# Optimization experiments

Hardware: AMD Instinct MI355X
Metric: run time of the kernel (lower is better)

## Reference

```python
import jax, jax.numpy as jnp
import numpy as np

B, R, C, S = 4, 64, 64, 32
V, E, H, L = 30000, 128, 128, 2


def setup_inputs() -> dict:
    key = jax.random.key(0)
    ks = jax.random.split(key, 8)
    return {
        "x": jax.random.randint(ks[0], (B, R, C, S), 0, V),
        "embed": jax.random.normal(ks[1], (V, E), jnp.float32) * 0.02,
        "W_ih": jax.random.normal(ks[2], (L, H, H), jnp.float32) * 0.05,
        "W_hh": jax.random.normal(ks[3], (L, H, H), jnp.float32) * 0.05,
        "b_ih": jax.random.normal(ks[4], (L, H), jnp.float32) * 0.05,
        "b_hh": jax.random.normal(ks[5], (L, H), jnp.float32) * 0.05,
        "pred_W": jax.random.normal(ks[6], (1, 2 * H), jnp.float32) * 0.05,
        "pred_b": jax.random.normal(ks[7], (1,), jnp.float32) * 0.05,
    }


def _rnn_last(x_seq, W_ih, W_hh, b_ih, b_hh):
    """Multi-layer elman RNN (relu), batch_first. x_seq: [N,S,E] -> last hidden of top layer [N,H]."""
    N = x_seq.shape[0]
    inp = x_seq
    for l in range(W_ih.shape[0]):  # small fixed layer loop
        Wi, Wh, bi, bh = W_ih[l], W_hh[l], b_ih[l], b_hh[l]
        # precompute input projection for all timesteps: [N,S,H]
        pre = jnp.einsum('nse,he->nsh', inp, Wi) + bi

        def step(h, p_t):
            h = jax.nn.relu(p_t + h @ Wh.T + bh)
            return h, h

        h0 = jnp.zeros((N, Wh.shape[0]), inp.dtype)
        _, hs = jax.lax.scan(step, h0, jnp.swapaxes(pre, 0, 1))  # [S,N,H]
        inp = jnp.swapaxes(hs, 0, 1)  # [N,S,H]
    return inp[:, -1, :]


def reference(x, embed, W_ih, W_hh, b_ih, b_hh, pred_W, pred_b):
    Bb, Rr, Cc, Ss = x.shape
    emb = embed[x]  # [B,R,C,S,E]  (dropout is identity in eval mode)
    h = _rnn_last(emb.reshape(Bb * Rr * Cc, Ss, emb.shape[-1]), W_ih, W_hh, b_ih, b_hh)
    h = h.reshape(Bb, Rr, Cc, -1)  # per-cell hidden; h_n[-1] == output[:,-1,:] of top layer
    # H_global[cell] = sum over same-row cells (excl self) + same-col cells (excl self)
    Hg = h.sum(axis=2, keepdims=True) + h.sum(axis=1, keepdims=True) - 2.0 * h
    feat = jnp.concatenate([h, Hg], axis=-1)  # [B,R,C,2H]
    return (feat @ pred_W.T + pred_b)[..., 0]  # [B,R,C]
```

## Files before the change

### kernel.cpp

```cpp
#include <hip/hip_runtime.h>
#include <hip/hip_bf16.h>


typedef __attribute__((ext_vector_type(8))) short short8;
typedef __attribute__((ext_vector_type(4))) float f32x4;
typedef __attribute__((ext_vector_type(2))) unsigned int u32x2;
typedef __attribute__((ext_vector_type(4))) unsigned int u32x4;

#define Hd 128
#define Sd 32
#define VROWS 30000

__device__ __forceinline__ unsigned short f2b(float f) {
  __hip_bfloat16 h = __float2bfloat16(f);
  return reinterpret_cast<unsigned short&>(h);
}
__device__ __forceinline__ unsigned int pack2(float a, float b) {
  return (unsigned int)f2b(a) | ((unsigned int)f2b(b) << 16);
}
__device__ __forceinline__ float blo(unsigned int u) { return __uint_as_float(u << 16); }
__device__ __forceinline__ float bhi(unsigned int u) { return __uint_as_float(u & 0xffff0000u); }

__device__ __forceinline__ f32x4 mfma16(short8 a, short8 b, f32x4 c) {
  return __builtin_amdgcn_mfma_f32_16x16x32_bf16(a, b, c, 0, 0, 0);
}

__device__ __forceinline__ short8 load_row8_bf16(const float* __restrict__ p) {
  const float4* q = reinterpret_cast<const float4*>(p);
  float4 a = q[0], b = q[1];
  short8 s;
  s[0] = (short)f2b(a.x); s[1] = (short)f2b(a.y);
  s[2] = (short)f2b(a.z); s[3] = (short)f2b(a.w);
  s[4] = (short)f2b(b.x); s[5] = (short)f2b(b.y);
  s[6] = (short)f2b(b.z); s[7] = (short)f2b(b.w);
  return s;
}

__global__ __launch_bounds__(256, 1) void k_t1p(const float* __restrict__ embed,
                                                const float* __restrict__ W_ih,
                                                const float* __restrict__ b_ih,
                                                const float* __restrict__ b_hh,
                                                unsigned int* __restrict__ T1p) {
  const int tid = threadIdx.x, lane = tid & 63, wid = tid >> 6;
  const int l15 = lane & 15, lg = lane >> 4;
  const int gw = blockIdx.x * 4 + wid;

  short8 Wf[8][4];
  f32x4 biasD[8];
#pragma unroll
  for (int m = 0; m < 8; ++m) {
#pragma unroll
    for (int kt = 0; kt < 4; ++kt)
      Wf[m][kt] = load_row8_bf16(W_ih + (16 * m + l15) * Hd + 32 * kt + 8 * lg);
    const float4 bi = *reinterpret_cast<const float4*>(b_ih + 16 * m + 4 * lg);
    const float4 bh = *reinterpret_cast<const float4*>(b_hh + 16 * m + 4 * lg);
    biasD[m] = (f32x4){bi.x + bh.x, bi.y + bh.y, bi.z + bh.z, bi.w + bh.w};
  }

  for (int tt = gw; tt < 1875; tt += 1024) {
    const int v = tt * 16 + l15;
    short8 Ef[4];
#pragma unroll
    for (int kt = 0; kt < 4; ++kt)
      Ef[kt] = load_row8_bf16(embed + (size_t)v * Hd + 32 * kt + 8 * lg);
    f32x4 acc[8];
#pragma unroll
    for (int m = 0; m < 8; ++m) acc[m] = biasD[m];
#pragma unroll
    for (int kt = 0; kt < 4; ++kt)
#pragma unroll
      for (int m = 0; m < 8; ++m) acc[m] = mfma16(Wf[m][kt], Ef[kt], acc[m]);
    unsigned int dw[16];
#pragma unroll
    for (int m = 0; m < 8; ++m) {
      dw[2 * m]     = pack2(acc[m][0], acc[m][1]);
      dw[2 * m + 1] = pack2(acc[m][2], acc[m][3]);
    }
    unsigned int* dst = T1p + (size_t)v * 64 + lg * 16;
#pragma unroll
    for (int j = 0; j < 4; ++j)
      *reinterpret_cast<u32x4*>(dst + 4 * j) =
          (u32x4){dw[4 * j], dw[4 * j + 1], dw[4 * j + 2], dw[4 * j + 3]};
  }
}

__global__ __launch_bounds__(256, 2) void k_rnn(
    const int* __restrict__ x, const unsigned int* __restrict__ T1p,
    const float* __restrict__ W_ih, const float* __restrict__ W_hh,
    const float* __restrict__ b_ih, const float* __restrict__ b_hh,
    const float* __restrict__ pred_W, float* __restrict__ sbuf) {
  __shared__ alignas(16) unsigned char slab[2][8192];
  __shared__ int xs[32 * 33 + 16];
  __shared__ float sred[4][32][2];

  const int tid = threadIdx.x, lane = tid & 63, ws = tid >> 6;
  const int l15 = lane & 15, lg = lane >> 4;
  const int seq0 = blockIdx.x * 32;

#pragma unroll
  for (int k = 0; k < 4; ++k) {
    int e = tid + k * 256;
    xs[(e >> 5) * 33 + (e & 31)] = x[(size_t)seq0 * Sd + e];
  }
  if (tid < 32) xs[tid * 33 + 32] = 0;
  __syncthreads();

  const int s0 = l15, s1 = l15 + 16;
  const int jbase = 16 * lg + 4 * ws;

  u32x2 t1q[2][2];
  {
    int i0 = xs[s0 * 33 + 0], i1 = xs[s1 * 33 + 0];
    const u32x2* p0 = reinterpret_cast<const u32x2*>(T1p + (size_t)i0 * 64 + jbase);
    const u32x2* p1 = reinterpret_cast<const u32x2*>(T1p + (size_t)i1 * 64 + jbase);
    t1q[0][0] = p0[0]; t1q[0][1] = p0[1];
    t1q[1][0] = p1[0]; t1q[1][1] = p1[1];
  }

  short8 Wh0[2][4], Wi1[2][4], Wh1[2][4];
#pragma unroll
  for (int mt = 0; mt < 2; ++mt)
#pragma unroll
    for (int kt = 0; kt < 4; ++kt) {
      const int ro = (32 * ws + 16 * mt + l15) * Hd + 32 * kt + 8 * lg;
      Wh0[mt][kt] = load_row8_bf16(W_hh + ro);
      Wi1[mt][kt] = load_row8_bf16(W_ih + 16384 + ro);
      Wh1[mt][kt] = load_row8_bf16(W_hh + 16384 + ro);
    }
  u32x2 bsumP[2];
#pragma unroll
  for (int mt = 0; mt < 2; ++mt) {
    const float4 bi = *reinterpret_cast<const float4*>(b_ih + Hd + 32 * ws + 16 * mt + 4 * lg);
    const float4 bh = *reinterpret_cast<const float4*>(b_hh + Hd + 32 * ws + 16 * mt + 4 * lg);
    bsumP[mt][0] = pack2(bi.x + bh.x, bi.y + bh.y);
    bsumP[mt][1] = pack2(bi.z + bh.z, bi.w + bh.w);
  }
  int wb[2][2], rb[2][4];
#pragma unroll
  for (int bt = 0; bt < 2; ++bt) {
#pragma unroll
    for (int mt = 0; mt < 2; ++mt)
      wb[bt][mt] = bt * 4096 + l15 * 256 + ((64 * ws + 32 * mt + 8 * lg) ^ (l15 << 4));
#pragma unroll
    for (int kt = 0; kt < 4; ++kt)
      rb[bt][kt] = bt * 4096 + l15 * 256 + ((64 * kt + 16 * lg) ^ (l15 << 4));
  }

  short8 h1f[2][4], h2f[2][4];
  f32x4 acc[2][2];

#pragma unroll
  for (int bt = 0; bt < 2; ++bt)
#pragma unroll
    for (int mt = 0; mt < 2; ++mt) {
      u32x2 q = t1q[bt][mt];
      float a0 = fmaxf(blo(q[0]), 0.f), a1 = fmaxf(bhi(q[0]), 0.f);
      float a2 = fmaxf(blo(q[1]), 0.f), a3 = fmaxf(bhi(q[1]), 0.f);
      u32x2 w; w[0] = pack2(a0, a1); w[1] = pack2(a2, a3);
      *reinterpret_cast<u32x2*>(slab[0] + wb[bt][mt]) = w;
    }
  {
    int i0 = xs[s0 * 33 + 1], i1 = xs[s1 * 33 + 1];
    const u32x2* p0 = reinterpret_cast<const u32x2*>(T1p + (size_t)i0 * 64 + jbase);
    const u32x2* p1 = reinterpret_cast<const u32x2*>(T1p + (size_t)i1 * 64 + jbase);
    t1q[0][0] = p0[0]; t1q[0][1] = p0[1];
    t1q[1][0] = p1[0]; t1q[1][1] = p1[1];
  }
  asm volatile("s_waitcnt lgkmcnt(0)" ::: "memory");
  __builtin_amdgcn_s_barrier();
#pragma unroll
  for (int bt = 0; bt < 2; ++bt)
#pragma unroll
    for (int kt = 0; kt < 4; ++kt)
      h1f[bt][kt] = *reinterpret_cast<const short8*>(slab[0] + rb[bt][kt]);

#pragma unroll
  for (int mt = 0; mt < 2; ++mt)
#pragma unroll
    for (int bt = 0; bt < 2; ++bt)
      acc[mt][bt] = (f32x4){blo(bsumP[mt][0]), bhi(bsumP[mt][0]),
                            blo(bsumP[mt][1]), bhi(bsumP[mt][1])};
#pragma unroll
  for (int kt = 0; kt < 4; ++kt)
#pragma unroll
    for (int mt = 0; mt < 2; ++mt)
#pragma unroll
      for (int bt = 0; bt < 2; ++bt)
        acc[mt][bt] = mfma16(Wi1[mt][kt], h1f[bt][kt], acc[mt][bt]);
#pragma unroll
  for (int bt = 0; bt < 2; ++bt)
#pragma unroll
    for (int mt = 0; mt < 2; ++mt) {
      f32x4 a = acc[mt][bt];
      u32x2 w;
      w[0] = pack2(fmaxf(a[0], 0.f), fmaxf(a[1], 0.f));
      w[1] = pack2(fmaxf(a[2], 0.f), fmaxf(a[3], 0.f));
      *reinterpret_cast<u32x2*>(slab[1] + wb[bt][mt]) = w;
    }
  asm volatile("s_waitcnt lgkmcnt(0)" ::: "memory");
  __builtin_amdgcn_s_barrier();
#pragma unroll
  for (int bt = 0; bt < 2; ++bt)
#pragma unroll
    for (int kt = 0; kt < 4; ++kt)
      h2f[bt][kt] = *reinterpret_cast<const short8*>(slab[1] + rb[bt][kt]);

#pragma unroll 1
  for (int t = 1; t < Sd; ++t) {
#pragma unroll
    for (int mt = 0; mt < 2; ++mt)
#pragma unroll
      for (int bt = 0; bt < 2; ++bt)
        acc[mt][bt] = mfma16(Wh0[mt][0], h1f[bt][0], (f32x4){0.f, 0.f, 0.f, 0.f});
#pragma unroll
    for (int kt = 1; kt < 4; ++kt)
#pragma unroll
      for (int mt = 0; mt < 2; ++mt)
#pragma unroll
        for (int bt = 0; bt < 2; ++bt)
          acc[mt][bt] = mfma16(Wh0[mt][kt], h1f[bt][kt], acc[mt][bt]);
#pragma unroll
    for (int bt = 0; bt < 2; ++bt)
#pragma unroll
      for (int mt = 0; mt < 2; ++mt) {
        u32x2 q = t1q[bt][mt];
        f32x4 a = acc[mt][bt];
        u32x2 w;
        w[0] = pack2(fmaxf(a[0] + blo(q[0]), 0.f), fmaxf(a[1] + bhi(q[0]), 0.f));
        w[1] = pack2(fmaxf(a[2] + blo(q[1]), 0.f), fmaxf(a[3] + bhi(q[1]), 0.f));
        *reinterpret_cast<u32x2*>(slab[0] + wb[bt][mt]) = w;
      }
    {
      int i0 = xs[s0 * 33 + t + 1], i1 = xs[s1 * 33 + t + 1];
      const u32x2* p0 = reinterpret_cast<const u32x2*>(T1p + (size_t)i0 * 64 + jbase);
      const u32x2* p1 = reinterpret_cast<const u32x2*>(T1p + (size_t)i1 * 64 + jbase);
      t1q[0][0] = p0[0]; t1q[0][1] = p0[1];
      t1q[1][0] = p1[0]; t1q[1][1] = p1[1];
    }
    asm volatile("s_waitcnt lgkmcnt(0)" ::: "memory");
    __builtin_amdgcn_s_barrier();
#pragma unroll
    for (int bt = 0; bt < 2; ++bt)
#pragma unroll
      for (int kt = 0; kt < 4; ++kt)
        h1f[bt][kt] = *reinterpret_cast<const short8*>(slab[0] + rb[bt][kt]);

#pragma unroll
    for (int mt = 0; mt < 2; ++mt)
#pragma unroll
      for (int bt = 0; bt < 2; ++bt)
        acc[mt][bt] = (f32x4){blo(bsumP[mt][0]), bhi(bsumP[mt][0]),
                              blo(bsumP[mt][1]), bhi(bsumP[mt][1])};
#pragma unroll
    for (int kt = 0; kt < 4; ++kt)
#pragma unroll
      for (int mt = 0; mt < 2; ++mt)
#pragma unroll
        for (int bt = 0; bt < 2; ++bt) {
          acc[mt][bt] = mfma16(Wi1[mt][kt], h1f[bt][kt], acc[mt][bt]);
          acc[mt][bt] = mfma16(Wh1[mt][kt], h2f[bt][kt], acc[mt][bt]);
        }
    if (t < Sd - 1) {
#pragma unroll
      for (int bt = 0; bt < 2; ++bt)
#pragma unroll
        for (int mt = 0; mt < 2; ++mt) {
          f32x4 a = acc[mt][bt];
          u32x2 w;
          w[0] = pack2(fmaxf(a[0], 0.f), fmaxf(a[1], 0.f));
          w[1] = pack2(fmaxf(a[2], 0.f), fmaxf(a[3], 0.f));
          *reinterpret_cast<u32x2*>(slab[1] + wb[bt][mt]) = w;
        }
      asm volatile("s_waitcnt lgkmcnt(0)" ::: "memory");
      __builtin_amdgcn_s_barrier();
#pragma unroll
      for (int bt = 0; bt < 2; ++bt)
#pragma unroll
        for (int kt = 0; kt < 4; ++kt)
          h2f[bt][kt] = *reinterpret_cast<const short8*>(slab[1] + rb[bt][kt]);
    }
  }

  float p1[2] = {0.f, 0.f}, p2[2] = {0.f, 0.f};
#pragma unroll
  for (int mt = 0; mt < 2; ++mt) {
    const float4 w1 = *reinterpret_cast<const float4*>(pred_W + 32 * ws + 16 * mt + 4 * lg);
    const float4 w2 = *reinterpret_cast<const float4*>(pred_W + Hd + 32 * ws + 16 * mt + 4 * lg);
#pragma unroll
    for (int bt = 0; bt < 2; ++bt) {
      f32x4 a = acc[mt][bt];
      float a0 = fmaxf(a[0], 0.f), a1 = fmaxf(a[1], 0.f);
      float a2 = fmaxf(a[2], 0.f), a3 = fmaxf(a[3], 0.f);
      p1[bt] += a0 * w1.x + a1 * w1.y + a2 * w1.z + a3 * w1.w;
      p2[bt] += a0 * w2.x + a1 * w2.y + a2 * w2.z + a3 * w2.w;
    }
  }
#pragma unroll
  for (int bt = 0; bt < 2; ++bt) {
    p1[bt] += __shfl_xor(p1[bt], 16); p1[bt] += __shfl_xor(p1[bt], 32);
    p2[bt] += __shfl_xor(p2[bt], 16); p2[bt] += __shfl_xor(p2[bt], 32);
  }
  if (lg == 0) {
#pragma unroll
    for (int bt = 0; bt < 2; ++bt) {
      sred[ws][bt * 16 + l15][0] = p1[bt];
      sred[ws][bt * 16 + l15][1] = p2[bt];
    }
  }
  __syncthreads();
  if (tid < 64) {
    int nl = tid >> 1, st = tid & 1;
    float v = sred[0][nl][st] + sred[1][nl][st] + sred[2][nl][st] + sred[3][nl][st];
    sbuf[st * 16384 + seq0 + nl] = v;
  }
}

__global__ __launch_bounds__(1024) void k_final(const float* __restrict__ sbuf,
                                                const float* __restrict__ pred_b,
                                                float* __restrict__ out) {
  __shared__ float s2s[64][65];
  __shared__ float rowS[64], colS[64];
  const int b = blockIdx.x, tid = threadIdx.x;
  const float* s1g = sbuf + b * 4096;
  const float* s2g = sbuf + 16384 + b * 4096;
#pragma unroll
  for (int i = 0; i < 4; ++i) {
    int j = tid + i * 1024;
    s2s[j >> 6][j & 63] = s2g[j];
  }
  __syncthreads();
  if (tid < 64) {
    float s = 0.f;
    for (int cc = 0; cc < 64; ++cc) s += s2s[tid][cc];
    rowS[tid] = s;
  } else if (tid < 128) {
    int cc = tid - 64;
    float s = 0.f;
    for (int r = 0; r < 64; ++r) s += s2s[r][cc];
    colS[cc] = s;
  }
  __syncthreads();
  const float pb = pred_b[0];
#pragma unroll
  for (int i = 0; i < 4; ++i) {
    int j = tid + i * 1024;
    int r = j >> 6, cc = j & 63;
    out[b * 4096 + j] = s1g[j] + rowS[r] + colS[cc] - 2.f * s2s[r][cc] + pb;
  }
}

extern "C" void kernel_launch(void* const* d_in, const int* in_sizes, int n_in,
                              void* d_out, int out_size, void* d_ws,
                              size_t ws_size, hipStream_t stream) {
  const int* x = (const int*)d_in[0];
  const float* embed = (const float*)d_in[1];
  const float* W_ih = (const float*)d_in[2];
  const float* W_hh = (const float*)d_in[3];
  const float* b_ih = (const float*)d_in[4];
  const float* b_hh = (const float*)d_in[5];
  const float* pred_W = (const float*)d_in[6];
  const float* pred_b = (const float*)d_in[7];

  unsigned int* T1p = (unsigned int*)d_ws;
  float* sbuf = (float*)((char*)d_ws + (size_t)VROWS * 256);
  float* out = (float*)d_out;

  k_t1p<<<256, 256, 0, stream>>>(embed, W_ih, b_ih, b_hh, T1p);
  k_rnn<<<512, 256, 0, stream>>>(x, T1p, W_ih, W_hh, b_ih, b_hh, pred_W, sbuf);
  k_final<<<4, 1024, 0, stream>>>(sbuf, pred_b, out);
}
```

Baseline: 146.6 us.

## Skew RNN layers into one barrier per timestep with double-buffered LDS

Restructures the two-layer recurrence so layer 0 at step t and layer 1 at step t-1 are computed in the same iteration and share a single barrier, instead of two barriers per step. Hidden states go to double-buffered LDS slabs, and the embedding-projection gather is prefetched two steps ahead. A final layer-1 step runs after the loop. This roughly halves the workgroup barriers on the serial critical path and hides gather latency, at the cost of more LDS and registers.

```diff
diff --git a/kernel.cpp b/kernel.cpp
--- a/kernel.cpp
+++ b/kernel.cpp
@@ -23,6 +23,13 @@
 
 __device__ __forceinline__ f32x4 mfma16(short8 a, short8 b, f32x4 c) {
   return __builtin_amdgcn_mfma_f32_16x16x32_bf16(a, b, c, 0, 0, 0);
+}
+
+__device__ __forceinline__ void phase_fence() {
+  asm volatile("s_waitcnt lgkmcnt(0)" ::: "memory");
+  __builtin_amdgcn_sched_barrier(0);
+  __builtin_amdgcn_s_barrier();
+  __builtin_amdgcn_sched_barrier(0);
 }
 
 __device__ __forceinline__ short8 load_row8_bf16(const float* __restrict__ p) {
@@ -89,7 +96,7 @@
     const float* __restrict__ W_ih, const float* __restrict__ W_hh,
     const float* __restrict__ b_ih, const float* __restrict__ b_hh,
     const float* __restrict__ pred_W, float* __restrict__ sbuf) {
-  __shared__ alignas(16) unsigned char slab[2][8192];
+  __shared__ alignas(16) unsigned char slab[2][2][8192];
   __shared__ int xs[32 * 33 + 16];
   __shared__ float sred[4][32][2];
 
@@ -102,19 +109,18 @@
     int e = tid + k * 256;
     xs[(e >> 5) * 33 + (e & 31)] = x[(size_t)seq0 * Sd + e];
   }
-  if (tid < 32) xs[tid * 33 + 32] = 0;
   __syncthreads();
 
   const int s0 = l15, s1 = l15 + 16;
   const int jbase = 16 * lg + 4 * ws;
 
-  u32x2 t1q[2][2];
+  u32x2 t1c[2][2], t1n[2][2];
   {
     int i0 = xs[s0 * 33 + 0], i1 = xs[s1 * 33 + 0];
     const u32x2* p0 = reinterpret_cast<const u32x2*>(T1p + (size_t)i0 * 64 + jbase);
     const u32x2* p1 = reinterpret_cast<const u32x2*>(T1p + (size_t)i1 * 64 + jbase);
-    t1q[0][0] = p0[0]; t1q[0][1] = p0[1];
-    t1q[1][0] = p1[0]; t1q[1][1] = p1[1];
+    t1c[0][0] = p0[0]; t1c[0][1] = p0[1];
+    t1c[1][0] = p1[0]; t1c[1][1] = p1[1];
   }
 
   short8 Wh0[2][4], Wi1[2][4], Wh1[2][4];
@@ -153,60 +159,40 @@
   for (int bt = 0; bt < 2; ++bt)
 #pragma unroll
     for (int mt = 0; mt < 2; ++mt) {
-      u32x2 q = t1q[bt][mt];
-      float a0 = fmaxf(blo(q[0]), 0.f), a1 = fmaxf(bhi(q[0]), 0.f);
-      float a2 = fmaxf(blo(q[1]), 0.f), a3 = fmaxf(bhi(q[1]), 0.f);
-      u32x2 w; w[0] = pack2(a0, a1); w[1] = pack2(a2, a3);
-      *reinterpret_cast<u32x2*>(slab[0] + wb[bt][mt]) = w;
+      u32x2 q = t1c[bt][mt];
+      u32x2 w;
+      w[0] = pack2(fmaxf(blo(q[0]), 0.f), fmaxf(bhi(q[0]), 0.f));
+      w[1] = pack2(fmaxf(blo(q[1]), 0.f), fmaxf(bhi(q[1]), 0.f));
+      *reinterpret_cast<u32x2*>(&slab[0][0][0] + wb[bt][mt]) = w;
+      *reinterpret_cast<u32x2*>(&slab[0][1][0] + wb[bt][mt]) = (u32x2){0u, 0u};
     }
   {
     int i0 = xs[s0 * 33 + 1], i1 = xs[s1 * 33 + 1];
     const u32x2* p0 = reinterpret_cast<const u32x2*>(T1p + (size_t)i0 * 64 + jbase);
     const u32x2* p1 = reinterpret_cast<const u32x2*>(T1p + (size_t)i1 * 64 + jbase);
-    t1q[0][0] = p0[0]; t1q[0][1] = p0[1];
-    t1q[1][0] = p1[0]; t1q[1][1] = p1[1];
-  }
-  asm volatile("s_waitcnt lgkmcnt(0)" ::: "memory");
-  __builtin_amdgcn_s_barrier();
+    t1c[0][0] = p0[0]; t1c[0][1] = p0[1];
+    t1c[1][0] = p1[0]; t1c[1][1] = p1[1];
+    int j0 = xs[s0 * 33 + 2], j1 = xs[s1 * 33 + 2];
+    const u32x2* q0 = reinterpret_cast<const u32x2*>(T1p + (size_t)j0 * 64 + jbase);
+    const u32x2* q1 = reinterpret_cast<const u32x2*>(T1p + (size_t)j1 * 64 + jbase);
+    t1n[0][0] = q0[0]; t1n[0][1] = q0[1];
+    t1n[1][0] = q1[0]; t1n[1][1] = q1[1];
+  }
+  phase_fence();
 #pragma unroll
   for (int bt = 0; bt < 2; ++bt)
 #pragma unroll
-    for (int kt = 0; kt < 4; ++kt)
-      h1f[bt][kt] = *reinterpret_cast<const short8*>(slab[0] + rb[bt][kt]);
-
-#pragma unroll
-  for (int mt = 0; mt < 2; ++mt)
-#pragma unroll
-    for (int bt = 0; bt < 2; ++bt)
-      acc[mt][bt] = (f32x4){blo(bsumP[mt][0]), bhi(bsumP[mt][0]),
-                            blo(bsumP[mt][1]), bhi(bsumP[mt][1])};
-#pragma unroll
-  for (int kt = 0; kt < 4; ++kt)
-#pragma unroll
-    for (int mt = 0; mt < 2; ++mt)
-#pragma unroll
-      for (int bt = 0; bt < 2; ++bt)
-        acc[mt][bt] = mfma16(Wi1[mt][kt], h1f[bt][kt], acc[mt][bt]);
-#pragma unroll
-  for (int bt = 0; bt < 2; ++bt)
-#pragma unroll
-    for (int mt = 0; mt < 2; ++mt) {
-      f32x4 a = acc[mt][bt];
-      u32x2 w;
-      w[0] = pack2(fmaxf(a[0], 0.f), fmaxf(a[1], 0.f));
-      w[1] = pack2(fmaxf(a[2], 0.f), fmaxf(a[3], 0.f));
-      *reinterpret_cast<u32x2*>(slab[1] + wb[bt][mt]) = w;
-    }
-  asm volatile("s_waitcnt lgkmcnt(0)" ::: "memory");
-  __builtin_amdgcn_s_barrier();
-#pragma unroll
-  for (int bt = 0; bt < 2; ++bt)
-#pragma unroll
-    for (int kt = 0; kt < 4; ++kt)
-      h2f[bt][kt] = *reinterpret_cast<const short8*>(slab[1] + rb[bt][kt]);
+    for (int kt = 0; kt < 4; ++kt) {
+      h1f[bt][kt] = *reinterpret_cast<const short8*>(&slab[0][0][0] + rb[bt][kt]);
+      h2f[bt][kt] = *reinterpret_cast<const short8*>(&slab[0][1][0] + rb[bt][kt]);
+    }
 
 #pragma unroll 1
   for (int t = 1; t < Sd; ++t) {
+    const int pn = t & 1;
+    unsigned char* w1s = &slab[pn][0][0];
+    unsigned char* w2s = &slab[pn][1][0];
+
 #pragma unroll
     for (int mt = 0; mt < 2; ++mt)
 #pragma unroll
@@ -223,27 +209,25 @@
     for (int bt = 0; bt < 2; ++bt)
 #pragma unroll
       for (int mt = 0; mt < 2; ++mt) {
-        u32x2 q = t1q[bt][mt];
+        u32x2 q = t1c[bt][mt];
         f32x4 a = acc[mt][bt];
         u32x2 w;
         w[0] = pack2(fmaxf(a[0] + blo(q[0]), 0.f), fmaxf(a[1] + bhi(q[0]), 0.f));
         w[1] = pack2(fmaxf(a[2] + blo(q[1]), 0.f), fmaxf(a[3] + bhi(q[1]), 0.f));
-        *reinterpret_cast<u32x2*>(slab[0] + wb[bt][mt]) = w;
+        *reinterpret_cast<u32x2*>(w1s + wb[bt][mt]) = w;
       }
+#pragma unroll
+    for (int bt = 0; bt < 2; ++bt)
+#pragma unroll
+      for (int mt = 0; mt < 2; ++mt) t1c[bt][mt] = t1n[bt][mt];
     {
-      int i0 = xs[s0 * 33 + t + 1], i1 = xs[s1 * 33 + t + 1];
+      const int tn = (t + 2 > 31) ? 31 : t + 2;
+      int i0 = xs[s0 * 33 + tn], i1 = xs[s1 * 33 + tn];
       const u32x2* p0 = reinterpret_cast<const u32x2*>(T1p + (size_t)i0 * 64 + jbase);
       const u32x2* p1 = reinterpret_cast<const u32x2*>(T1p + (size_t)i1 * 64 + jbase);
-      t1q[0][0] = p0[0]; t1q[0][1] = p0[1];
-      t1q[1][0] = p1[0]; t1q[1][1] = p1[1];
-    }
-    asm volatile("s_waitcnt lgkmcnt(0)" ::: "memory");
-    __builtin_amdgcn_s_barrier();
-#pragma unroll
-    for (int bt = 0; bt < 2; ++bt)
-#pragma unroll
-      for (int kt = 0; kt < 4; ++kt)
-        h1f[bt][kt] = *reinterpret_cast<const short8*>(slab[0] + rb[bt][kt]);
+      t1n[0][0] = p0[0]; t1n[0][1] = p0[1];
+      t1n[1][0] = p1[0]; t1n[1][1] = p1[1];
+    }
 
 #pragma unroll
     for (int mt = 0; mt < 2; ++mt)
@@ -260,26 +244,42 @@
           acc[mt][bt] = mfma16(Wi1[mt][kt], h1f[bt][kt], acc[mt][bt]);
           acc[mt][bt] = mfma16(Wh1[mt][kt], h2f[bt][kt], acc[mt][bt]);
         }
-    if (t < Sd - 1) {
-#pragma unroll
-      for (int bt = 0; bt < 2; ++bt)
-#pragma unroll
-        for (int mt = 0; mt < 2; ++mt) {
-          f32x4 a = acc[mt][bt];
-          u32x2 w;
-          w[0] = pack2(fmaxf(a[0], 0.f), fmaxf(a[1], 0.f));
-          w[1] = pack2(fmaxf(a[2], 0.f), fmaxf(a[3], 0.f));
-          *reinterpret_cast<u32x2*>(slab[1] + wb[bt][mt]) = w;
-        }
-      asm volatile("s_waitcnt lgkmcnt(0)" ::: "memory");
-      __builtin_amdgcn_s_barrier();
-#pragma unroll
-      for (int bt = 0; bt < 2; ++bt)
-#pragma unroll
-        for (int kt = 0; kt < 4; ++kt)
-          h2f[bt][kt] = *reinterpret_cast<const short8*>(slab[1] + rb[bt][kt]);
-    }
-  }
+#pragma unroll
+    for (int bt = 0; bt < 2; ++bt)
+#pragma unroll
+      for (int mt = 0; mt < 2; ++mt) {
+        f32x4 a = acc[mt][bt];
+        u32x2 w;
+        w[0] = pack2(fmaxf(a[0], 0.f), fmaxf(a[1], 0.f));
+        w[1] = pack2(fmaxf(a[2], 0.f), fmaxf(a[3], 0.f));
+        *reinterpret_cast<u32x2*>(w2s + wb[bt][mt]) = w;
+      }
+
+    phase_fence();
+#pragma unroll
+    for (int bt = 0; bt < 2; ++bt)
+#pragma unroll
+      for (int kt = 0; kt < 4; ++kt) {
+        h1f[bt][kt] = *reinterpret_cast<const short8*>(w1s + rb[bt][kt]);
+        h2f[bt][kt] = *reinterpret_cast<const short8*>(w2s + rb[bt][kt]);
+      }
+  }
+
+#pragma unroll
+  for (int mt = 0; mt < 2; ++mt)
+#pragma unroll
+    for (int bt = 0; bt < 2; ++bt)
+      acc[mt][bt] = (f32x4){blo(bsumP[mt][0]), bhi(bsumP[mt][0]),
+                            blo(bsumP[mt][1]), bhi(bsumP[mt][1])};
+#pragma unroll
+  for (int kt = 0; kt < 4; ++kt)
+#pragma unroll
+    for (int mt = 0; mt < 2; ++mt)
+#pragma unroll
+      for (int bt = 0; bt < 2; ++bt) {
+        acc[mt][bt] = mfma16(Wi1[mt][kt], h1f[bt][kt], acc[mt][bt]);
+        acc[mt][bt] = mfma16(Wh1[mt][kt], h2f[bt][kt], acc[mt][bt]);
+      }
 
   float p1[2] = {0.f, 0.f}, p2[2] = {0.f, 0.f};
 #pragma unroll
```

New measurement: 148.2 us. Within noise of the previous version (+1.1%).
